# Kernel tuning notes

Measured on AMD Instinct MI355X. Metric: run time of the kernel, lower is better.

The kernel has to match this reference:

```python
import math
import jax, jax.numpy as jnp
import numpy as np

N_HEAD = 12
HEAD_DIM = 64
NEG = -1e9

def setup_inputs() -> dict:
    key = jax.random.key(0)
    k1, k2, k3 = jax.random.split(key, 3)
    B, T, C = 16, 1024, 768
    x = jax.random.normal(k1, (B, T, C), dtype=jnp.float32)
    attention_mask = jnp.ones((B, T), dtype=jnp.int32)
    W_attn = jax.random.normal(k2, (C, 3 * C), dtype=jnp.float32) * 0.02
    b_attn = jnp.zeros((3 * C,), dtype=jnp.float32)
    W_proj = jax.random.normal(k3, (C, C), dtype=jnp.float32) * 0.02
    b_proj = jnp.zeros((C,), dtype=jnp.float32)
    return {"x": x, "attention_mask": attention_mask, "W_attn": W_attn,
            "b_attn": b_attn, "W_proj": W_proj, "b_proj": b_proj}

def reference(x, attention_mask, W_attn, b_attn, W_proj, b_proj):
    B, T, C = x.shape
    H, D = N_HEAD, HEAD_DIM
    qkv = x @ W_attn + b_attn                       # [B,T,3C]
    q, k, v = jnp.split(qkv, 3, axis=-1)
    q = q.reshape(B, T, H, D).transpose(0, 2, 1, 3)  # [B,H,T,D]
    k = k.reshape(B, T, H, D).transpose(0, 2, 1, 3)
    v = v.reshape(B, T, H, D).transpose(0, 2, 1, 3)
    att = jnp.einsum('bhqd,bhkd->bhqk', q, k) / math.sqrt(D)  # [B,H,T,T]
    causal = jnp.tril(jnp.ones((T, T), dtype=bool))[None, None]
    key_mask = (attention_mask[:, None, None, :] != 0)          # [B,1,1,T]
    # masked_fill(-inf) then replace inf with -1e9 == set masked to -1e9
    att = jnp.where(causal & key_mask, att, NEG)
    att = jax.nn.softmax(att, axis=-1)
    query_mask = attention_mask[:, None, :, None].astype(att.dtype)  # [B,1,T,1]
    att = att * query_mask
    y = jnp.einsum('bhqk,bhkd->bhqd', att, v)        # [B,H,T,D]
    y = y.transpose(0, 2, 1, 3).reshape(B, T, C)
    return y @ W_proj + b_proj
```

## Files before the change

kernel.cpp:

```cpp
#include <hip/hip_runtime.h>
#include <stdint.h>

typedef unsigned short u16;
typedef unsigned int u32;
typedef __attribute__((ext_vector_type(8))) short short8;
typedef __attribute__((ext_vector_type(4))) float f32x4;
typedef __attribute__((ext_vector_type(4))) unsigned short u16x4;

#define LDS_AS __attribute__((address_space(3)))
#define GLB_AS __attribute__((address_space(1)))

__device__ __forceinline__ u16 f2bf(float f) {
  u32 u = __float_as_uint(f);
  u = (u + 0x7FFFu + ((u >> 16) & 1u)) >> 16;
  return (u16)u;
}

__device__ __forceinline__ void gload_lds16(const u16* g, u16* l) {
  __builtin_amdgcn_global_load_lds((const GLB_AS u32*)g, (LDS_AS u32*)l, 16, 0, 0);
}

__device__ __forceinline__ f32x4 mfma16(short8 a, short8 b, f32x4 c) {
  return __builtin_amdgcn_mfma_f32_16x16x32_bf16(a, b, c, 0, 0, 0);
}

__global__ __launch_bounds__(256) void k_cvt(const float* __restrict__ in,
                                             u16* __restrict__ out, int n4) {
  int i = blockIdx.x * 256 + threadIdx.x;
  if (i >= n4) return;
  f32x4 v = ((const f32x4*)in)[i];
  u16x4 o = {f2bf(v[0]), f2bf(v[1]), f2bf(v[2]), f2bf(v[3])};
  ((u16x4*)out)[i] = o;
}

__global__ __launch_bounds__(256) void k_transpose_cvt(const float* __restrict__ W,
                                                       u16* __restrict__ Wt, int K, int N) {
  __shared__ float tile[32][33];
  int n0 = blockIdx.x * 32;
  int k0 = blockIdx.y * 32;
  int tx = threadIdx.x & 31, ty = threadIdx.x >> 5;
#pragma unroll
  for (int i = 0; i < 4; i++) {
    int k = k0 + ty + i * 8;
    tile[ty + i * 8][tx] = W[(size_t)k * N + n0 + tx];
  }
  __syncthreads();
#pragma unroll
  for (int i = 0; i < 4; i++) {
    int n = n0 + ty + i * 8;
    Wt[(size_t)n * K + k0 + tx] = f2bf(tile[tx][ty + i * 8]);
  }
}

template <int MODE>
__global__ __launch_bounds__(256) void k_gemm(const u16* __restrict__ A,
                                              const u16* __restrict__ Bt,
                                              const float* __restrict__ bias,
                                              void* __restrict__ C, u16* __restrict__ vTo,
                                              int M, int N, int K) {
  __shared__ __align__(16) u16 As[2][128 * 32];
  __shared__ __align__(16) u16 Bs[2][128 * 32];
  const int nwg = gridDim.x;
  const int wgo = blockIdx.x;
  const int cpx = nwg >> 3;
  const int swz = (wgo & 7) * cpx + (wgo >> 3);
  const int ntn = N >> 7;
  const int tm = swz / ntn, tn = swz % ntn;
  const int m0 = tm << 7, n0 = tn << 7;
  const int tid = threadIdx.x;
  const int lane = tid & 63, w = tid >> 6;
  const int wm = (w >> 1) << 6, wn = (w & 1) << 6;
  const int fr = lane & 15, kg = lane >> 4;

  f32x4 acc[4][4];
#pragma unroll
  for (int i = 0; i < 4; i++)
#pragma unroll
    for (int j = 0; j < 4; j++) acc[i][j] = (f32x4){0.f, 0.f, 0.f, 0.f};

  const int rs = tid >> 2;
  const int ckq = (((tid & 3) ^ (rs & 3) ^ ((tid >> 4) & 1)) << 3);
  const u16* ga = A + (size_t)(m0 + rs) * K + ckq;
  const u16* gb = Bt + (size_t)(n0 + rs) * K + ckq;
  const size_t row64 = (size_t)64 * K;

#define GSTAGE(buf, kt)                                              \
  {                                                                  \
    const int ko = (kt) * 32;                                        \
    gload_lds16(ga + ko, &As[buf][tid * 8]);                         \
    gload_lds16(ga + row64 + ko, &As[buf][2048 + tid * 8]);          \
    gload_lds16(gb + ko, &Bs[buf][tid * 8]);                         \
    gload_lds16(gb + row64 + ko, &Bs[buf][2048 + tid * 8]);          \
  }

  const int KT = K >> 5;
  GSTAGE(0, 0);

  const int cs = ((kg ^ (fr & 3) ^ ((fr >> 2) & 1)) << 3);

  for (int kt = 0; kt < KT; ++kt) {
    const int cur = kt & 1;
    if (kt + 1 < KT) {
      GSTAGE(cur ^ 1, kt + 1);
      asm volatile("s_waitcnt vmcnt(4)" ::: "memory");
    } else {
      asm volatile("s_waitcnt vmcnt(0)" ::: "memory");
    }
    __builtin_amdgcn_sched_barrier(0);
    __builtin_amdgcn_s_barrier();
    __builtin_amdgcn_sched_barrier(0);

    short8 af[4], bf[4];
#pragma unroll
    for (int mi = 0; mi < 4; mi++)
      af[mi] = *(const short8*)&As[cur][(wm + mi * 16 + fr) * 32 + cs];
#pragma unroll
    for (int nj = 0; nj < 4; nj++)
      bf[nj] = *(const short8*)&Bs[cur][(wn + nj * 16 + fr) * 32 + cs];
    asm volatile("s_waitcnt lgkmcnt(0)" ::: "memory");
    __builtin_amdgcn_sched_barrier(0);
#pragma unroll
    for (int mi = 0; mi < 4; mi++)
#pragma unroll
      for (int nj = 0; nj < 4; nj++)
        acc[mi][nj] = mfma16(af[mi], bf[nj], acc[mi][nj]);

    __builtin_amdgcn_sched_barrier(0);
    __builtin_amdgcn_s_barrier();
  }
#undef GSTAGE

  const int r0 = (lane >> 4) << 2;
  const bool isv = (MODE == 1) && (n0 >= 1536);
#pragma unroll
  for (int mi = 0; mi < 4; mi++) {
    const int row = m0 + wm + mi * 16 + r0;
#pragma unroll
    for (int nj = 0; nj < 4; nj++) {
      const int col = n0 + wn + nj * 16 + fr;
      const float bs = bias[col];
      f32x4 v = acc[mi][nj];
      if (MODE == 0) {
#pragma unroll
        for (int r = 0; r < 4; r++)
          ((float*)C)[(size_t)(row + r) * N + col] = v[r] + bs;
      } else if (!isv) {
#pragma unroll
        for (int r = 0; r < 4; r++)
          ((u16*)C)[(size_t)(row + r) * 1536 + col] = f2bf(v[r] + bs);
      } else {
        int d = col - 1536;
        int hh = d >> 6, dd = d & 63;
        int bb = row >> 10, t = row & 1023;
        u16x4 pk = {f2bf(v[0] + bs), f2bf(v[1] + bs), f2bf(v[2] + bs), f2bf(v[3] + bs)};
        *(u16x4*)&vTo[((size_t)(bb * 12 + hh) * 64 + dd) * 1024 + t] = pk;
      }
    }
  }
}

__global__ __launch_bounds__(256, 3) void k_attn(const u16* __restrict__ qk,
                                                 const u16* __restrict__ vT,
                                                 const int* __restrict__ amask,
                                                 u16* __restrict__ y) {
  __shared__ __align__(16) u16 Ks[2][64 * 64];
  __shared__ __align__(16) u16 Vs[2][64 * 64];
  __shared__ __align__(16) u16 Ps[4][2][16 * 72];
  __shared__ u32 mbits[32];

  const int bh = blockIdx.x;
  const int qp = blockIdx.y;
  const int b = bh / 12, h = bh % 12;
  const int qbA = qp * 64, qbB = (15 - qp) * 64;
  const int nt = 16 - qp;
  const int tid = threadIdx.x, lane = tid & 63, w = tid >> 6;
  const int fr = lane & 15, kg = lane >> 4;

  const u16* qg = qk + (size_t)b * 1024 * 1536 + h * 64;
  const u16* kgp = qg + 768;
  const u16* vg = vT + (size_t)bh * 64 * 1024;
  const int* mrow = amask + b * 1024;

  short8 qfA[2], qfB[2];
  {
    const u16* ra = qg + (size_t)(qbA + w * 16 + fr) * 1536 + kg * 8;
    const u16* rb = qg + (size_t)(qbB + w * 16 + fr) * 1536 + kg * 8;
    qfA[0] = *(const short8*)ra;
    qfA[1] = *(const short8*)(ra + 32);
    qfB[0] = *(const short8*)rb;
    qfB[1] = *(const short8*)(rb + 32);
  }

#pragma unroll
  for (int i = 0; i < 4; i++) {
    int tok = i * 256 + tid;
    unsigned long long bm = __ballot(mrow[tok] != 0);
    if (lane == 0) {
      int base = (i * 256 + w * 64) >> 5;
      mbits[base] = (u32)bm;
      mbits[base + 1] = (u32)(bm >> 32);
    }
  }
  __syncthreads();

  const int sr0 = tid >> 3, sc = tid & 7;
  const int sr1 = sr0 + 32;
  const int sw0 = (sc ^ (sr0 & 7)) << 3;

#define STAGE_KV(buf, kv0)                                                          \
  {                                                                                 \
    gload_lds16(kgp + (size_t)((kv0) + sr0) * 1536 + sw0, &Ks[buf][tid * 8]);       \
    gload_lds16(kgp + (size_t)((kv0) + sr1) * 1536 + sw0, &Ks[buf][2048 + tid * 8]);\
    gload_lds16(vg + (size_t)sr0 * 1024 + (kv0) + sw0, &Vs[buf][tid * 8]);          \
    gload_lds16(vg + (size_t)sr1 * 1024 + (kv0) + sw0, &Vs[buf][2048 + tid * 8]);   \
  }

  STAGE_KV(0, 0);

  f32x4 oA[4], oB[4];
  float psA[4], psB[4];
#pragma unroll
  for (int i = 0; i < 4; i++) {
    oA[i] = (f32x4){0.f, 0.f, 0.f, 0.f};
    oB[i] = (f32x4){0.f, 0.f, 0.f, 0.f};
    psA[i] = 0.f;
    psB[i] = 0.f;
  }
  u16* PwA = &Ps[w][0][0];
  u16* PwB = &Ps[w][1][0];

  const float SCALE2 = 0.125f * 1.44269504f;
  const float MFIX = 4.0f;

  for (int it = 0; it < nt; ++it) {
    const int kv0 = it * 64;
    const int cur = it & 1;
    if (it + 1 < nt) {
      STAGE_KV(cur ^ 1, kv0 + 64);
      asm volatile("s_waitcnt vmcnt(4)" ::: "memory");
    } else {
      asm volatile("s_waitcnt vmcnt(0)" ::: "memory");
    }
    __builtin_amdgcn_sched_barrier(0);
    __builtin_amdgcn_s_barrier();
    __builtin_amdgcn_sched_barrier(0);

    const bool aAct = (it <= qp);
    const u16* Kc = Ks[cur];
    const u16* Vc = Vs[cur];

    f32x4 sA[4], sB[4];
#pragma unroll
    for (int nf = 0; nf < 4; nf++) {
      sA[nf] = (f32x4){0.f, 0.f, 0.f, 0.f};
      sB[nf] = (f32x4){0.f, 0.f, 0.f, 0.f};
    }
#pragma unroll
    for (int nf = 0; nf < 4; nf++) {
      const int base = (nf * 16 + fr) * 64;
      short8 k0 = *(const short8*)&Kc[base + ((kg ^ (fr & 7)) << 3)];
      short8 k1 = *(const short8*)&Kc[base + (((kg + 4) ^ (fr & 7)) << 3)];
      sB[nf] = mfma16(qfB[0], k0, sB[nf]);
      sB[nf] = mfma16(qfB[1], k1, sB[nf]);
      if (aAct) {
        sA[nf] = mfma16(qfA[0], k0, sA[nf]);
        sA[nf] = mfma16(qfA[1], k1, sA[nf]);
      }
    }

    float kmof[4];
#pragma unroll
    for (int nf = 0; nf < 4; nf++) {
      int kv = kv0 + nf * 16 + fr;
      u32 wv = mbits[kv >> 5];
      kmof[nf] = ((wv >> (kv & 31)) & 1u) ? -MFIX : -1e9f;
    }

    auto softmax = [&](f32x4(&s)[4], float(&ps)[4], u16* Pw, int qb, bool diag) {
#pragma unroll
      for (int nf = 0; nf < 4; nf++)
#pragma unroll
        for (int r = 0; r < 4; r++) {
          float v = fmaf(s[nf][r], SCALE2, kmof[nf]);
          if (diag) {
            int kv = kv0 + nf * 16 + fr;
            int q = qb + w * 16 + kg * 4 + r;
            if (kv > q) v = -1e9f;
          }
          float e = exp2f(v);
          ps[r] += e;
          Pw[(kg * 4 + r) * 72 + nf * 16 + fr] = f2bf(e);
        }
    };

    if (aAct) softmax(sA, psA, PwA, qbA, it == qp);
    softmax(sB, psB, PwB, qbB, it == nt - 1);

#pragma unroll
    for (int kc = 0; kc < 2; kc++) {
      short8 pB = *(const short8*)&PwB[fr * 72 + kc * 32 + kg * 8];
      short8 pA;
      if (aAct) pA = *(const short8*)&PwA[fr * 72 + kc * 32 + kg * 8];
#pragma unroll
      for (int df = 0; df < 4; df++) {
        short8 vf = *(const short8*)&Vc[(df * 16 + fr) * 64 + (((kc * 4 + kg) ^ (fr & 7)) << 3)];
        oB[df] = mfma16(pB, vf, oB[df]);
        if (aAct) oA[df] = mfma16(pA, vf, oA[df]);
      }
    }

    __builtin_amdgcn_sched_barrier(0);
    __builtin_amdgcn_s_barrier();
  }
#undef STAGE_KV

#pragma unroll
  for (int r = 0; r < 4; r++) {
    float lAr = psA[r];
    lAr += __shfl_xor(lAr, 1);
    lAr += __shfl_xor(lAr, 2);
    lAr += __shfl_xor(lAr, 4);
    lAr += __shfl_xor(lAr, 8);
    float lBr = psB[r];
    lBr += __shfl_xor(lBr, 1);
    lBr += __shfl_xor(lBr, 2);
    lBr += __shfl_xor(lBr, 4);
    lBr += __shfl_xor(lBr, 8);
    int qA = qbA + w * 16 + kg * 4 + r;
    int qB = qbB + w * 16 + kg * 4 + r;
    float nA = ((mbits[qA >> 5] >> (qA & 31)) & 1u) ? (1.f / lAr) : 0.f;
    float nB = ((mbits[qB >> 5] >> (qB & 31)) & 1u) ? (1.f / lBr) : 0.f;
#pragma unroll
    for (int df = 0; df < 4; df++) {
      y[(size_t)(b * 1024 + qA) * 768 + h * 64 + df * 16 + fr] = f2bf(oA[df][r] * nA);
      y[(size_t)(b * 1024 + qB) * 768 + h * 64 + df * 16 + fr] = f2bf(oB[df][r] * nB);
    }
  }
}

extern "C" void kernel_launch(void* const* d_in, const int* in_sizes, int n_in,
                              void* d_out, int out_size, void* d_ws, size_t ws_size,
                              hipStream_t stream) {
  const float* x = (const float*)d_in[0];
  const int* amask = (const int*)d_in[1];
  const float* W_attn = (const float*)d_in[2];
  const float* b_attn = (const float*)d_in[3];
  const float* W_proj = (const float*)d_in[4];
  const float* b_proj = (const float*)d_in[5];
  float* out = (float*)d_out;

  u16* xb = (u16*)d_ws;
  u16* wta = xb + (size_t)16384 * 768;
  u16* wtp = wta + (size_t)2304 * 768;
  u16* qk = wtp + (size_t)768 * 768;
  u16* vT = qk + (size_t)16384 * 1536;
  u16* yb = vT + (size_t)192 * 64 * 1024;

  (void)in_sizes; (void)n_in; (void)out_size; (void)ws_size;

  k_cvt<<<(16384 * 768 / 4) / 256, 256, 0, stream>>>(x, xb, 16384 * 768 / 4);
  k_transpose_cvt<<<dim3(2304 / 32, 768 / 32), 256, 0, stream>>>(W_attn, wta, 768, 2304);
  k_transpose_cvt<<<dim3(768 / 32, 768 / 32), 256, 0, stream>>>(W_proj, wtp, 768, 768);

  k_gemm<1><<<(16384 / 128) * (2304 / 128), 256, 0, stream>>>(xb, wta, b_attn, qk, vT,
                                                              16384, 2304, 768);
  k_attn<<<dim3(192, 8), 256, 0, stream>>>(qk, vT, amask, yb);
  k_gemm<0><<<(16384 / 128) * (768 / 128), 256, 0, stream>>>(yb, wtp, b_proj, out, nullptr,
                                                             16384, 768, 768);
}
```

Measured before the change: 206.4 us.

## Load K and V fragments directly from global memory instead of LDS staging

The attention kernel stops staging K and V tiles into double-buffered shared memory with async global-to-LDS loads. Each wave now reads its MFMA K and V fragments straight from global memory (relying on the caches), which removes the per-iteration block barriers and the LDS footprint, and drops the occupancy hint from launch bounds. In exchange, each of the four waves re-fetches the same K/V data from global memory with no explicit prefetch, so load latency is exposed and cache traffic rises.

Result: slower. 281.9 us (+36.6%).

```diff
diff --git a/kernel.cpp b/kernel.cpp
--- a/kernel.cpp
+++ b/kernel.cpp
@@ -159,12 +159,10 @@
   }
 }
 
-__global__ __launch_bounds__(256, 3) void k_attn(const u16* __restrict__ qk,
-                                                 const u16* __restrict__ vT,
-                                                 const int* __restrict__ amask,
-                                                 u16* __restrict__ y) {
-  __shared__ __align__(16) u16 Ks[2][64 * 64];
-  __shared__ __align__(16) u16 Vs[2][64 * 64];
+__global__ __launch_bounds__(256) void k_attn(const u16* __restrict__ qk,
+                                              const u16* __restrict__ vT,
+                                              const int* __restrict__ amask,
+                                              u16* __restrict__ y) {
   __shared__ __align__(16) u16 Ps[4][2][16 * 72];
   __shared__ u32 mbits[32];
 
@@ -203,20 +201,6 @@
   }
   __syncthreads();
 
-  const int sr0 = tid >> 3, sc = tid & 7;
-  const int sr1 = sr0 + 32;
-  const int sw0 = (sc ^ (sr0 & 7)) << 3;
-
-#define STAGE_KV(buf, kv0)                                                          \
-  {                                                                                 \
-    gload_lds16(kgp + (size_t)((kv0) + sr0) * 1536 + sw0, &Ks[buf][tid * 8]);       \
-    gload_lds16(kgp + (size_t)((kv0) + sr1) * 1536 + sw0, &Ks[buf][2048 + tid * 8]);\
-    gload_lds16(vg + (size_t)sr0 * 1024 + (kv0) + sw0, &Vs[buf][tid * 8]);          \
-    gload_lds16(vg + (size_t)sr1 * 1024 + (kv0) + sw0, &Vs[buf][2048 + tid * 8]);   \
-  }
-
-  STAGE_KV(0, 0);
-
   f32x4 oA[4], oB[4];
   float psA[4], psB[4];
 #pragma unroll
@@ -234,20 +218,7 @@
 
   for (int it = 0; it < nt; ++it) {
     const int kv0 = it * 64;
-    const int cur = it & 1;
-    if (it + 1 < nt) {
-      STAGE_KV(cur ^ 1, kv0 + 64);
-      asm volatile("s_waitcnt vmcnt(4)" ::: "memory");
-    } else {
-      asm volatile("s_waitcnt vmcnt(0)" ::: "memory");
-    }
-    __builtin_amdgcn_sched_barrier(0);
-    __builtin_amdgcn_s_barrier();
-    __builtin_amdgcn_sched_barrier(0);
-
     const bool aAct = (it <= qp);
-    const u16* Kc = Ks[cur];
-    const u16* Vc = Vs[cur];
 
     f32x4 sA[4], sB[4];
 #pragma unroll
@@ -257,9 +228,9 @@
     }
 #pragma unroll
     for (int nf = 0; nf < 4; nf++) {
-      const int base = (nf * 16 + fr) * 64;
-      short8 k0 = *(const short8*)&Kc[base + ((kg ^ (fr & 7)) << 3)];
-      short8 k1 = *(const short8*)&Kc[base + (((kg + 4) ^ (fr & 7)) << 3)];
+      const u16* kp = kgp + (size_t)(kv0 + nf * 16 + fr) * 1536 + kg * 8;
+      short8 k0 = *(const short8*)kp;
+      short8 k1 = *(const short8*)(kp + 32);
       sB[nf] = mfma16(qfB[0], k0, sB[nf]);
       sB[nf] = mfma16(qfB[1], k1, sB[nf]);
       if (aAct) {
@@ -303,16 +274,12 @@
       if (aAct) pA = *(const short8*)&PwA[fr * 72 + kc * 32 + kg * 8];
 #pragma unroll
       for (int df = 0; df < 4; df++) {
-        short8 vf = *(const short8*)&Vc[(df * 16 + fr) * 64 + (((kc * 4 + kg) ^ (fr & 7)) << 3)];
+        short8 vf = *(const short8*)&vg[(size_t)(df * 16 + fr) * 1024 + kv0 + kc * 32 + kg * 8];
         oB[df] = mfma16(pB, vf, oB[df]);
         if (aAct) oA[df] = mfma16(pA, vf, oA[df]);
       }
     }
-
-    __builtin_amdgcn_sched_barrier(0);
-    __builtin_amdgcn_s_barrier();
-  }
-#undef STAGE_KV
+  }
 
 #pragma unroll
   for (int r = 0; r < 4; r++) {
```
